# Optimization experiments

Hardware: AMD Instinct MI355X
Metric: run time of the kernel (lower is better)

Reference implementation:

```python
import jax, jax.numpy as jnp
import numpy as np

B, S, DIN, DOUT = 4, 2048, 4096, 4096

def setup_inputs() -> dict:
    key = jax.random.key(0)
    k1, k2, k3, k4 = jax.random.split(key, 4)
    x = jax.random.normal(k1, (B, S, DIN), dtype=jnp.float32)
    # int8-valued quantized weights in [-127, 127]
    weight_int8 = jax.random.randint(k2, (DOUT, DIN), -127, 128, dtype=jnp.int32).astype(jnp.int8)
    # per-output-row scales, positive, clamped at 1e-8 like the torch code
    weight_scale = jnp.maximum(jax.random.uniform(k3, (DOUT, 1), dtype=jnp.float32) * 0.01, 1e-8)
    bias = jax.random.normal(k4, (DOUT,), dtype=jnp.float32)
    return {"x": x, "weight_int8": weight_int8, "weight_scale": weight_scale, "bias": bias}

def reference(x, weight_int8, weight_scale, bias):
    # Dequantize: [DOUT, DIN] = int8 * per-row scale (broadcast over in_features)
    w = weight_int8.astype(x.dtype) * weight_scale.astype(x.dtype)
    # F.linear: y = x @ w.T + bias
    return jnp.einsum('bsd,od->bso', x, w) + bias
```

## Files before the change

kernel.cpp:

```cpp
#include <hip/hip_runtime.h>
#include <hip/hip_bf16.h>
#include <stdint.h>

#define MM 8192
#define NN 4096
#define KK 4096
#define BM 128
#define BN 128
#define BK 32

typedef short bf16x8 __attribute__((ext_vector_type(8)));
typedef float f32x4 __attribute__((ext_vector_type(4)));

__device__ __forceinline__ unsigned int f2bf(float f) {
    unsigned int u = __builtin_bit_cast(unsigned int, f);
    u += 0x7FFFu + ((u >> 16) & 1u);
    return u >> 16;
}

__global__ __launch_bounds__(256) void cvt_x_kernel(const float* __restrict__ x,
                                                    unsigned short* __restrict__ xb) {
    int i = blockIdx.x * blockDim.x + threadIdx.x;
    const float4* p = (const float4*)x + (size_t)i * 2;
    float4 a = p[0], b = p[1];
    uint4 o;
    o.x = f2bf(a.x) | (f2bf(a.y) << 16);
    o.y = f2bf(a.z) | (f2bf(a.w) << 16);
    o.z = f2bf(b.x) | (f2bf(b.y) << 16);
    o.w = f2bf(b.z) | (f2bf(b.w) << 16);
    ((uint4*)xb)[i] = o;
}

__global__ __launch_bounds__(256) void cvt_w_kernel(const int* __restrict__ w,
                                                    unsigned short* __restrict__ wb) {
    int i = blockIdx.x * blockDim.x + threadIdx.x;
    const int4* p = (const int4*)w + (size_t)i * 2;
    int4 a = p[0], b = p[1];
    uint4 o;
    o.x = f2bf((float)a.x) | (f2bf((float)a.y) << 16);
    o.y = f2bf((float)a.z) | (f2bf((float)a.w) << 16);
    o.z = f2bf((float)b.x) | (f2bf((float)b.y) << 16);
    o.w = f2bf((float)b.z) | (f2bf((float)b.w) << 16);
    ((uint4*)wb)[i] = o;
}

__global__ __launch_bounds__(256) void gemm_kernel(const unsigned short* __restrict__ A,
                                                   const unsigned short* __restrict__ Bt,
                                                   const float* __restrict__ scale,
                                                   const float* __restrict__ bias,
                                                   float* __restrict__ C) {
    __shared__ __align__(16) unsigned short As[BM * BK];
    __shared__ __align__(16) unsigned short Bs[BN * BK];

    const int nbn = NN / BN;
    const int nwg = (MM / BM) * nbn;
    const int cpx = nwg >> 3;
    int bid = blockIdx.x;
    int swz = (bid & 7) * cpx + (bid >> 3);
    const int bm = swz / nbn;
    const int bn = swz % nbn;

    const int tid  = threadIdx.x;
    const int lane = tid & 63;
    const int wid  = tid >> 6;
    const int wr   = wid >> 1;
    const int wc   = wid & 1;

    const int r  = lane & 15;
    const int kg = lane >> 4;

    f32x4 acc[4][4] = {};

    const size_t rowA0 = (size_t)bm * BM;
    const size_t rowB0 = (size_t)bn * BN;

    for (int k0 = 0; k0 < KK; k0 += BK) {
#pragma unroll
        for (int i = 0; i < 2; ++i) {
            int slot = i * 256 + tid;
            int row  = slot >> 2;
            int ch   = slot & 3;
            const unsigned short* gA = A  + (rowA0 + row) * KK + k0 + ch * 8;
            const unsigned short* gB = Bt + (rowB0 + row) * KK + k0 + ch * 8;
            unsigned short* lA = As + (size_t)(i * 256 + (wid << 6)) * 8;
            unsigned short* lB = Bs + (size_t)(i * 256 + (wid << 6)) * 8;
            __builtin_amdgcn_global_load_lds(
                (const __attribute__((address_space(1))) unsigned int*)gA,
                (__attribute__((address_space(3))) unsigned int*)lA, 16, 0, 0);
            __builtin_amdgcn_global_load_lds(
                (const __attribute__((address_space(1))) unsigned int*)gB,
                (__attribute__((address_space(3))) unsigned int*)lB, 16, 0, 0);
        }
        __syncthreads();

        bf16x8 af[4], bfr[4];
#pragma unroll
        for (int m = 0; m < 4; ++m)
            af[m] = *(const bf16x8*)&As[(wr * 64 + m * 16 + r) * BK + kg * 8];
#pragma unroll
        for (int n = 0; n < 4; ++n)
            bfr[n] = *(const bf16x8*)&Bs[(wc * 64 + n * 16 + r) * BK + kg * 8];
#pragma unroll
        for (int m = 0; m < 4; ++m)
#pragma unroll
            for (int n = 0; n < 4; ++n)
                acc[m][n] = __builtin_amdgcn_mfma_f32_16x16x32_bf16(af[m], bfr[n],
                                                                    acc[m][n], 0, 0, 0);
        __syncthreads();
    }

    const int rj = lane >> 4;
#pragma unroll
    for (int n = 0; n < 4; ++n) {
        int col  = bn * BN + wc * 64 + n * 16 + r;
        float sc = scale[col];
        float bi = bias[col];
#pragma unroll
        for (int m = 0; m < 4; ++m) {
            int row = bm * BM + wr * 64 + m * 16 + rj * 4;
#pragma unroll
            for (int j = 0; j < 4; ++j) {
                C[(size_t)(row + j) * NN + col] = acc[m][n][j] * sc + bi;
            }
        }
    }
}

extern "C" void kernel_launch(void* const* d_in, const int* in_sizes, int n_in,
                              void* d_out, int out_size, void* d_ws, size_t ws_size,
                              hipStream_t stream) {
    const float* x     = (const float*)d_in[0];
    const int*   w8    = (const int*)d_in[1];
    const float* scale = (const float*)d_in[2];
    const float* bias  = (const float*)d_in[3];
    float* out = (float*)d_out;

    unsigned short* xb = (unsigned short*)d_ws;
    unsigned short* wb = xb + (size_t)MM * KK;

    cvt_x_kernel<<<(MM * KK) / 2048, 256, 0, stream>>>(x, xb);
    cvt_w_kernel<<<(NN * KK) / 2048, 256, 0, stream>>>(w8, wb);
    gemm_kernel<<<(MM / BM) * (NN / BN), 256, 0, stream>>>(xb, wb, scale, bias, out);
}
```

Baseline: 601.6 us.

## Rewrite GEMM with 256x256 tiles, double-buffered LDS and interleaved quadrant pipeline

Replaces the 128x128x32 single-buffered GEMM with a 256x256x64 tile on 512 threads. LDS is double-buffered and XOR-swizzled, and global-to-LDS loads are staged in quarter-tile pieces interleaved with four MFMA quadrant phases, using explicit waitcnt, barriers and setprio. The aim is to hide load latency, raise arithmetic intensity and cut LDS bank conflicts. In exchange it needs 128 KB of LDS and many accumulator registers per thread, which may limit occupancy, and the hand-written waitcnt ordering is fragile.

```diff
diff --git a/kernel.cpp b/kernel.cpp
--- a/kernel.cpp
+++ b/kernel.cpp
@@ -1,13 +1,14 @@
 #include <hip/hip_runtime.h>
-#include <hip/hip_bf16.h>
 #include <stdint.h>
 
 #define MM 8192
 #define NN 4096
 #define KK 4096
-#define BM 128
-#define BN 128
-#define BK 32
+#define BM 256
+#define BN 256
+#define BK 64
+#define NT (KK / BK)
+#define NHALF (4 * NT)
 
 typedef short bf16x8 __attribute__((ext_vector_type(8)));
 typedef float f32x4 __attribute__((ext_vector_type(4)));
@@ -44,86 +45,164 @@
     ((uint4*)wb)[i] = o;
 }
 
-__global__ __launch_bounds__(256) void gemm_kernel(const unsigned short* __restrict__ A,
-                                                   const unsigned short* __restrict__ Bt,
-                                                   const float* __restrict__ scale,
-                                                   const float* __restrict__ bias,
-                                                   float* __restrict__ C) {
-    __shared__ __align__(16) unsigned short As[BM * BK];
-    __shared__ __align__(16) unsigned short Bs[BN * BK];
+#define SWZ(q) ((q) ^ ((((q) >> 9) & 3) << 5))
+
+__global__ __launch_bounds__(512, 2) void gemm_kernel(const unsigned short* __restrict__ A,
+                                                      const unsigned short* __restrict__ Bt,
+                                                      const float* __restrict__ scale,
+                                                      const float* __restrict__ bias,
+                                                      float* __restrict__ C) {
+    __shared__ __align__(16) unsigned short As[2][BM * BK];
+    __shared__ __align__(16) unsigned short Bs[2][BN * BK];
 
     const int nbn = NN / BN;
-    const int nwg = (MM / BM) * nbn;
-    const int cpx = nwg >> 3;
+    const int cpx = ((MM / BM) * (NN / BN)) >> 3;
     int bid = blockIdx.x;
-    int swz = (bid & 7) * cpx + (bid >> 3);
-    const int bm = swz / nbn;
-    const int bn = swz % nbn;
+    int swzb = (bid & 7) * cpx + (bid >> 3);
+    const int bm = swzb / nbn;
+    const int bn = swzb % nbn;
 
     const int tid  = threadIdx.x;
     const int lane = tid & 63;
     const int wid  = tid >> 6;
-    const int wr   = wid >> 1;
-    const int wc   = wid & 1;
-
-    const int r  = lane & 15;
-    const int kg = lane >> 4;
-
-    f32x4 acc[4][4] = {};
+    const int wm   = wid >> 2;
+    const int wn   = wid & 3;
+    const int r    = lane & 15;
+    const int kg   = lane >> 4;
 
     const size_t rowA0 = (size_t)bm * BM;
     const size_t rowB0 = (size_t)bn * BN;
 
-    for (int k0 = 0; k0 < KK; k0 += BK) {
-#pragma unroll
-        for (int i = 0; i < 2; ++i) {
-            int slot = i * 256 + tid;
-            int row  = slot >> 2;
-            int ch   = slot & 3;
-            const unsigned short* gA = A  + (rowA0 + row) * KK + k0 + ch * 8;
-            const unsigned short* gB = Bt + (rowB0 + row) * KK + k0 + ch * 8;
-            unsigned short* lA = As + (size_t)(i * 256 + (wid << 6)) * 8;
-            unsigned short* lB = Bs + (size_t)(i * 256 + (wid << 6)) * 8;
-            __builtin_amdgcn_global_load_lds(
-                (const __attribute__((address_space(1))) unsigned int*)gA,
-                (__attribute__((address_space(3))) unsigned int*)lA, 16, 0, 0);
-            __builtin_amdgcn_global_load_lds(
-                (const __attribute__((address_space(1))) unsigned int*)gB,
-                (__attribute__((address_space(3))) unsigned int*)lB, 16, 0, 0);
+    f32x4 acc[8][4] = {};
+    bf16x8 a[4][2], b0[2][2], b1[2][2];
+
+#define STAGE(hid_) do {                                                          \
+    int hh = (hid_);                                                              \
+    if (hh < NHALF) {                                                             \
+        int tt = hh >> 2, h4 = hh & 3;                                            \
+        int isA = (h4 == 0) || (h4 == 3);                                         \
+        int hi  = (h4 >= 2) ? 1 : 0;                                              \
+        int bo  = (tt & 1) * (BM * BK * 2);                                       \
+        const unsigned short* gb = isA ? A : Bt;                                  \
+        size_t row0 = isA ? rowA0 : rowB0;                                        \
+        char* lbase = (isA ? (char*)As : (char*)Bs) + bo + (hi << 14);            \
+        _Pragma("unroll")                                                         \
+        for (int ii = 0; ii < 2; ++ii) {                                          \
+            int q  = (hi << 14) + (ii * 512 + tid) * 16;                          \
+            int qs = SWZ(q);                                                      \
+            int rw = qs >> 7, cb = qs & 127;                                      \
+            const unsigned short* gs = gb + (row0 + rw) * KK + tt * BK + (cb >> 1); \
+            char* ld = lbase + (ii * 512 + (wid << 6)) * 16;                      \
+            __builtin_amdgcn_global_load_lds(                                     \
+                (const __attribute__((address_space(1))) unsigned int*)gs,        \
+                (__attribute__((address_space(3))) unsigned int*)ld, 16, 0, 0);   \
+        }                                                                         \
+    }                                                                             \
+} while (0)
+
+#define READ_A(mh_) do {                                                          \
+    _Pragma("unroll")                                                             \
+    for (int i_ = 0; i_ < 4; ++i_)                                                \
+        _Pragma("unroll")                                                         \
+        for (int s_ = 0; s_ < 2; ++s_) {                                          \
+            int rw = (mh_) * 128 + wm * 64 + i_ * 16 + r;                         \
+            int q  = rw * 128 + s_ * 64 + kg * 16;                                \
+            a[i_][s_] = *(const bf16x8*)((char*)As + bufo + SWZ(q));              \
+        }                                                                         \
+} while (0)
+
+#define READ_B(nh_, dst_) do {                                                    \
+    _Pragma("unroll")                                                             \
+    for (int j_ = 0; j_ < 2; ++j_)                                                \
+        _Pragma("unroll")                                                         \
+        for (int s_ = 0; s_ < 2; ++s_) {                                          \
+            int rw = (nh_) * 128 + wn * 32 + j_ * 16 + r;                         \
+            int q  = rw * 128 + s_ * 64 + kg * 16;                                \
+            dst_[j_][s_] = *(const bf16x8*)((char*)Bs + bufo + SWZ(q));           \
+        }                                                                         \
+} while (0)
+
+#define MFMA_Q(mh_, nh_, B_) do {                                                 \
+    _Pragma("unroll")                                                             \
+    for (int i_ = 0; i_ < 4; ++i_)                                                \
+        _Pragma("unroll")                                                         \
+        for (int j_ = 0; j_ < 2; ++j_)                                            \
+            _Pragma("unroll")                                                     \
+            for (int s_ = 0; s_ < 2; ++s_)                                        \
+                acc[(mh_) * 4 + i_][(nh_) * 2 + j_] =                             \
+                    __builtin_amdgcn_mfma_f32_16x16x32_bf16(                      \
+                        a[i_][s_], B_[j_][s_], acc[(mh_) * 4 + i_][(nh_) * 2 + j_], 0, 0, 0); \
+} while (0)
+
+    STAGE(0); STAGE(1); STAGE(2); STAGE(3);
+    asm volatile("s_waitcnt vmcnt(4)");
+    STAGE(4); STAGE(5); STAGE(6);
+    asm volatile("s_waitcnt vmcnt(6)");
+    __builtin_amdgcn_s_barrier();
+
+    for (int t = 0; t < NT; ++t) {
+        const int bufo = (t & 1) * (BM * BK * 2);
+
+        READ_A(0);
+        READ_B(0, b0);
+        STAGE(4 * t + 7);
+        asm volatile("s_waitcnt lgkmcnt(8)");
+        __builtin_amdgcn_s_barrier();
+        asm volatile("s_waitcnt lgkmcnt(0)");
+        __builtin_amdgcn_s_setprio(1);
+        MFMA_Q(0, 0, b0);
+        __builtin_amdgcn_s_setprio(0);
+        __builtin_amdgcn_s_barrier();
+
+        READ_B(1, b1);
+        STAGE(4 * t + 8);
+        __builtin_amdgcn_s_barrier();
+        asm volatile("s_waitcnt lgkmcnt(0)");
+        __builtin_amdgcn_s_setprio(1);
+        MFMA_Q(0, 1, b1);
+        __builtin_amdgcn_s_setprio(0);
+        __builtin_amdgcn_s_barrier();
+
+        READ_A(1);
+        STAGE(4 * t + 9);
+        __builtin_amdgcn_s_barrier();
+        asm volatile("s_waitcnt lgkmcnt(0)");
+        __builtin_amdgcn_s_setprio(1);
+        MFMA_Q(1, 1, b1);
+        __builtin_amdgcn_s_setprio(0);
+        __builtin_amdgcn_s_barrier();
+
+        STAGE(4 * t + 10);
+        __builtin_amdgcn_s_barrier();
+        __builtin_amdgcn_s_setprio(1);
+        MFMA_Q(1, 0, b0);
+        __builtin_amdgcn_s_setprio(0);
+        if (t < NT - 1) {
+            if (t == NT - 2) asm volatile("s_waitcnt vmcnt(0)");
+            else             asm volatile("s_waitcnt vmcnt(6)");
+            __builtin_amdgcn_s_barrier();
         }
-        __syncthreads();
-
-        bf16x8 af[4], bfr[4];
-#pragma unroll
-        for (int m = 0; m < 4; ++m)
-            af[m] = *(const bf16x8*)&As[(wr * 64 + m * 16 + r) * BK + kg * 8];
-#pragma unroll
-        for (int n = 0; n < 4; ++n)
-            bfr[n] = *(const bf16x8*)&Bs[(wc * 64 + n * 16 + r) * BK + kg * 8];
-#pragma unroll
-        for (int m = 0; m < 4; ++m)
-#pragma unroll
-            for (int n = 0; n < 4; ++n)
-                acc[m][n] = __builtin_amdgcn_mfma_f32_16x16x32_bf16(af[m], bfr[n],
-                                                                    acc[m][n], 0, 0, 0);
-        __syncthreads();
     }
 
     const int rj = lane >> 4;
 #pragma unroll
-    for (int n = 0; n < 4; ++n) {
-        int col  = bn * BN + wc * 64 + n * 16 + r;
+    for (int nj = 0; nj < 4; ++nj) {
+        int col  = bn * BN + (nj >> 1) * 128 + wn * 32 + (nj & 1) * 16 + r;
         float sc = scale[col];
         float bi = bias[col];
 #pragma unroll
-        for (int m = 0; m < 4; ++m) {
-            int row = bm * BM + wr * 64 + m * 16 + rj * 4;
+        for (int mi = 0; mi < 8; ++mi) {
+            int row = bm * BM + (mi >> 2) * 128 + wm * 64 + (mi & 3) * 16 + rj * 4;
 #pragma unroll
             for (int j = 0; j < 4; ++j) {
-                C[(size_t)(row + j) * NN + col] = acc[m][n][j] * sc + bi;
+                C[(size_t)(row + j) * NN + col] = acc[mi][nj][j] * sc + bi;
             }
         }
     }
+#undef STAGE
+#undef READ_A
+#undef READ_B
+#undef MFMA_Q
 }
 
 extern "C" void kernel_launch(void* const* d_in, const int* in_sizes, int n_in,
@@ -140,5 +219,5 @@
 
     cvt_x_kernel<<<(MM * KK) / 2048, 256, 0, stream>>>(x, xb);
     cvt_w_kernel<<<(NN * KK) / 2048, 256, 0, stream>>>(w8, wb);
-    gemm_kernel<<<(MM / BM) * (NN / BN), 256, 0, stream>>>(xb, wb, scale, bias, out);
-}
+    gemm_kernel<<<(MM / BM) * (NN / BN), 512, 0, stream>>>(xb, wb, scale, bias, out);
+}
```

Result: faster. 567.1 us (-5.7%).
